# Kernel optimization log

Hardware: AMD Instinct MI355X
Metric: run time of the kernel (lower is better)

## Reference

```python
import jax, jax.numpy as jnp
import numpy as np

E = 1024
H = 16
D = E // H  # head_dim = 64


def setup_inputs() -> dict:
    key = jax.random.key(0)
    k_x, k_w1, k_b1, k_w2, k_b2 = jax.random.split(key, 5)
    s = 1.0 / np.sqrt(E)
    return {
        "x": jax.random.normal(k_x, (2, 2048, E), dtype=jnp.float32),
        "qkv_w": jax.random.uniform(k_w1, (3 * E, E), jnp.float32, -s, s),
        "qkv_b": jax.random.uniform(k_b1, (3 * E,), jnp.float32, -s, s),
        "out_w": jax.random.uniform(k_w2, (E, E), jnp.float32, -s, s),
        "out_b": jax.random.uniform(k_b2, (E,), jnp.float32, -s, s),
    }


def reference(x, qkv_w, qkv_b, out_w, out_b):
    B, T, _ = x.shape
    # qkv projection (torch Linear: x @ W.T + b)
    qkv = x @ qkv_w.T + qkv_b  # [B, T, 3E]
    q, k, v = jnp.split(qkv, 3, axis=-1)
    # [B, T, E] -> [B, H, T, D]
    def to_heads(t):
        return t.reshape(B, T, H, D).transpose(0, 2, 1, 3)
    q, k, v = to_heads(q), to_heads(k), to_heads(v)
    scale = 1.0 / np.sqrt(D).astype(np.float32)
    scores = jnp.einsum("bhqd,bhkd->bhqk", q, k) * scale  # [B, H, T, T]
    attn = jax.nn.softmax(scores, axis=-1)
    # dropout is identity in eval mode
    out = jnp.einsum("bhqk,bhkd->bhqd", attn, v)  # [B, H, T, D]
    out = out.transpose(0, 2, 1, 3).reshape(B, T, E)
    return out @ out_w.T + out_b
```

## Files before the change

kernel.cpp:

```cpp
#include <hip/hip_runtime.h>

#define TT 2048
#define BB 2
#define EE 1024
#define HH 16
#define DD 64
#define E3 3072
#define NTOK 4096

typedef unsigned short u16;
typedef _Float16 __attribute__((ext_vector_type(8))) half8;
typedef _Float16 __attribute__((ext_vector_type(4))) half4;
typedef __fp16 __attribute__((ext_vector_type(2))) fp16x2;
typedef __attribute__((ext_vector_type(4))) float f32x4;

__device__ __forceinline__ unsigned f2h(float f) {
    union { _Float16 h; u16 u; } v; v.h = (_Float16)f; return (unsigned)v.u;
}
__device__ __forceinline__ fp16x2 pk2(float a, float b) {
    return __builtin_amdgcn_cvt_pkrtz(a, b);
}

__device__ __forceinline__ void async_ld16(const u16* g, const u16* l) {
    auto gp = reinterpret_cast<const __attribute__((address_space(1))) unsigned*>(
        reinterpret_cast<uintptr_t>(g));
    auto lp = reinterpret_cast<__attribute__((address_space(3))) unsigned*>(
        reinterpret_cast<uintptr_t>(l));
    __builtin_amdgcn_global_load_lds(gp, lp, 16, 0, 0);
}

__global__ __launch_bounds__(256) void split3(
    const float* __restrict__ x, const float* __restrict__ w1,
    const float* __restrict__ w2,
    u16* __restrict__ xh, u16* __restrict__ w1h, u16* __restrict__ w2h)
{
    const int N1 = (NTOK * EE) / 4;
    const int N2 = N1 + (E3 * EE) / 4;
    int i = blockIdx.x * 256 + threadIdx.x;
    const float* src; u16* dst; int j;
    if (i < N1)      { src = x;  dst = xh;  j = i; }
    else if (i < N2) { src = w1; dst = w1h; j = i - N1; }
    else             { src = w2; dst = w2h; j = i - N2; }
    float4 v = ((const float4*)src)[j];
    *(uint2*)&dst[(size_t)j * 4] = make_uint2(
        f2h(v.x) | (f2h(v.y) << 16), f2h(v.z) | (f2h(v.w) << 16));
}

__global__ __launch_bounds__(256) void vtrans(
    const u16* __restrict__ qkv, u16* __restrict__ vt)
{
    __shared__ u16 L[64][72];
    const int tid = threadIdx.x;
    const int t0 = blockIdx.x * 64;
    const int h  = blockIdx.y;
    const int b  = blockIdx.z;
    const int row = tid >> 2;
    const int c16 = (tid & 3) << 4;

    const u16* src = qkv + (size_t)(b * TT + t0 + row) * E3 + 2 * EE + h * DD + c16;
    *(uint4*)&L[row][c16]     = *(const uint4*)src;
    *(uint4*)&L[row][c16 + 8] = *(const uint4*)(src + 8);
    __syncthreads();

    union { uint4 u[2]; u16 s[16]; } P;
#pragma unroll
    for (int j = 0; j < 16; ++j) P.s[j] = L[c16 + j][row];
    u16* dst = vt + ((size_t)(b * HH + h) * DD + row) * TT + t0 + c16;
    *(uint4*)dst       = P.u[0];
    *(uint4*)(dst + 8) = P.u[1];
}

template <int WMT, bool QSCALE, bool F16OUT>
__global__ __launch_bounds__(256, 3) void gemm_f16(
    const u16* __restrict__ Ag, const u16* __restrict__ Wg,
    const float* __restrict__ bias, void* __restrict__ Cout, int M, int N)
{
    constexpr int BM = WMT * 32;
    constexpr int APASS = BM / 32;
    __shared__ u16 sA[BM * 64];
    __shared__ u16 sB[128 * 64];

    const int tid  = threadIdx.x;
    const int lane = tid & 63;
    const int wave = tid >> 6;
    const int quad = lane >> 4;
    const int l16  = lane & 15;
    const int wm = wave >> 1, wn = wave & 1;
    const int m0 = blockIdx.y * BM;
    const int n0 = blockIdx.x * 128;

    const int srow = tid >> 3;
    const int schk = tid & 7;

    const u16* ag[APASS]; int aldw[APASS];
#pragma unroll
    for (int p = 0; p < APASS; ++p) {
        int row = p * 32 + srow;
        ag[p] = Ag + (size_t)(m0 + row) * EE + ((schk ^ (row & 7)) << 3);
        aldw[p] = (p * 256 + wave * 64) * 8;
    }
    const u16* bg[4]; int bldw[4];
#pragma unroll
    for (int p = 0; p < 4; ++p) {
        int row = p * 32 + srow;
        bg[p] = Wg + (size_t)(n0 + row) * EE + ((schk ^ (row & 7)) << 3);
        bldw[p] = (p * 256 + wave * 64) * 8;
    }

    f32x4 acc[WMT][4];
#pragma unroll
    for (int mt = 0; mt < WMT; ++mt)
#pragma unroll
        for (int nt = 0; nt < 4; ++nt) acc[mt][nt] = (f32x4){0.f, 0.f, 0.f, 0.f};

    for (int k0 = 0; k0 < EE; k0 += 64) {
        __syncthreads();
#pragma unroll
        for (int p = 0; p < APASS; ++p) async_ld16(ag[p] + k0, sA + aldw[p]);
#pragma unroll
        for (int p = 0; p < 4; ++p)    async_ld16(bg[p] + k0, sB + bldw[p]);
        __syncthreads();

        half8 fa[WMT][2], fb[4][2];
#pragma unroll
        for (int mt = 0; mt < WMT; ++mt) {
            int r = wm * (WMT * 16) + mt * 16 + l16;
#pragma unroll
            for (int ks = 0; ks < 2; ++ks)
                fa[mt][ks] = *(const half8*)&sA[r * 64 + (((ks * 4 + quad) ^ (r & 7)) << 3)];
        }
#pragma unroll
        for (int nt = 0; nt < 4; ++nt) {
            int r = wn * 64 + nt * 16 + l16;
#pragma unroll
            for (int ks = 0; ks < 2; ++ks)
                fb[nt][ks] = *(const half8*)&sB[r * 64 + (((ks * 4 + quad) ^ (r & 7)) << 3)];
        }
#pragma unroll
        for (int ks = 0; ks < 2; ++ks)
#pragma unroll
            for (int mt = 0; mt < WMT; ++mt)
#pragma unroll
                for (int nt = 0; nt < 4; ++nt)
                    acc[mt][nt] = __builtin_amdgcn_mfma_f32_16x16x32_f16(
                        fa[mt][ks], fb[nt][ks], acc[mt][nt], 0, 0, 0);
    }

    const float scale = (QSCALE && n0 < EE) ? 0.18033688011112042f : 1.0f;
    float bv[4];
#pragma unroll
    for (int nt = 0; nt < 4; ++nt) bv[nt] = bias[n0 + wn * 64 + nt * 16 + l16];
#pragma unroll
    for (int mt = 0; mt < WMT; ++mt)
#pragma unroll
        for (int nt = 0; nt < 4; ++nt)
#pragma unroll
            for (int r = 0; r < 4; ++r) {
                int rg = m0 + wm * (WMT * 16) + mt * 16 + quad * 4 + r;
                int cg = n0 + wn * 64 + nt * 16 + l16;
                float v = (acc[mt][nt][r] + bv[nt]) * scale;
                if (F16OUT) ((u16*)Cout)[(size_t)rg * N + cg] = (u16)f2h(v);
                else        ((float*)Cout)[(size_t)rg * N + cg] = v;
            }
}

__global__ __launch_bounds__(256, 2) void attn_mfma(
    const u16* __restrict__ qkv, const u16* __restrict__ vt,
    u16* __restrict__ obuf)
{
    __shared__ u16 KB[2][128][64];
    __shared__ u16 VB[2][64][128];

    const int tid  = threadIdx.x;
    const int wave = tid >> 6;
    const int lane = tid & 63;
    const int quad = lane >> 4;
    const int l16  = lane & 15;

    const int q0 = blockIdx.x * 128;
    const int hh = blockIdx.y;
    const int b  = blockIdx.z;

    const int srow  = tid >> 3;
    const int schk  = tid & 7;
    const int vsrow = tid >> 4;
    const int vschk = tid & 15;
    const int ldsw  = wave * 512;

    half8 qb[2][2];
#pragma unroll
    for (int qt = 0; qt < 2; ++qt) {
        int row = q0 + wave * 32 + qt * 16 + l16;
        const u16* qg = qkv + (size_t)(b * TT + row) * E3 + hh * DD;
#pragma unroll
        for (int ks = 0; ks < 2; ++ks)
            qb[qt][ks] = *(const half8*)(qg + ks * 32 + quad * 8);
    }

#pragma unroll
    for (int p = 0; p < 4; ++p) {
        int krow = p * 32 + srow;
        async_ld16(qkv + (size_t)(b * TT + krow) * E3 + EE + hh * DD
                       + ((schk ^ (krow & 7)) << 3),
                   &KB[0][0][0] + p * 2048 + ldsw);
        int vrow = p * 16 + vsrow;
        async_ld16(vt + ((size_t)(b * HH + hh) * DD + vrow) * TT
                      + ((vschk ^ (vrow & 15)) << 3),
                   &VB[0][0][0] + p * 2048 + ldsw);
    }
    __syncthreads();

    const f32x4 Z = {0.f, 0.f, 0.f, 0.f};
    float l_i[2] = {0.f, 0.f};
    f32x4 o[4][2];
#pragma unroll
    for (int dt = 0; dt < 4; ++dt)
#pragma unroll
        for (int qt = 0; qt < 2; ++qt) o[dt][qt] = (f32x4){0.f, 0.f, 0.f, 0.f};

    int cur = 0;
    for (int kt = 0; kt < TT; kt += 128, cur ^= 1) {
        const int ktn = (kt + 128) & (TT - 1);
#pragma unroll
        for (int p = 0; p < 4; ++p) {
            int krow = p * 32 + srow;
            async_ld16(qkv + (size_t)(b * TT + ktn + krow) * E3 + EE + hh * DD
                           + ((schk ^ (krow & 7)) << 3),
                       &KB[cur ^ 1][0][0] + p * 2048 + ldsw);
            int vrow = p * 16 + vsrow;
            async_ld16(vt + ((size_t)(b * HH + hh) * DD + vrow) * TT + ktn
                          + ((vschk ^ (vrow & 15)) << 3),
                       &VB[cur ^ 1][0][0] + p * 2048 + ldsw);
        }

        half4 pb[2][8];
#pragma unroll
        for (int kg = 0; kg < 8; ++kg) {
            int r0 = kg * 16 + l16;
            half8 kf0 = *(const half8*)&KB[cur][r0][((quad)     ^ (r0 & 7)) << 3];
            half8 kf1 = *(const half8*)&KB[cur][r0][((4 + quad) ^ (r0 & 7)) << 3];
#pragma unroll
            for (int qt = 0; qt < 2; ++qt) {
                f32x4 t = __builtin_amdgcn_mfma_f32_16x16x32_f16(kf0, qb[qt][0], Z, 0, 0, 0);
                f32x4 s = __builtin_amdgcn_mfma_f32_16x16x32_f16(kf1, qb[qt][1], t, 0, 0, 0);
                float p0 = __builtin_amdgcn_exp2f(s[0]);
                float p1 = __builtin_amdgcn_exp2f(s[1]);
                float p2 = __builtin_amdgcn_exp2f(s[2]);
                float p3 = __builtin_amdgcn_exp2f(s[3]);
                l_i[qt] += (p0 + p1) + (p2 + p3);
                union { fp16x2 h[2]; half4 v; } u;
                u.h[0] = pk2(p0, p1);
                u.h[1] = pk2(p2, p3);
                pb[qt][kg] = u.v;
            }
        }

#pragma unroll
        for (int kg = 0; kg < 8; ++kg) {
            int c = kg * 2 + (quad >> 1);
#pragma unroll
            for (int dt = 0; dt < 4; ++dt) {
                int vr = dt * 16 + l16;
                half4 vf = *(const half4*)&VB[cur][vr]
                               [((c ^ l16) << 3) + ((quad & 1) << 2)];
                o[dt][0] = __builtin_amdgcn_mfma_f32_16x16x16f16(vf, pb[0][kg], o[dt][0], 0, 0, 0);
                o[dt][1] = __builtin_amdgcn_mfma_f32_16x16x16f16(vf, pb[1][kg], o[dt][1], 0, 0, 0);
            }
        }

        __syncthreads();
    }

    float inv[2];
#pragma unroll
    for (int qt = 0; qt < 2; ++qt) {
        float l = l_i[qt];
        l += __shfl_xor(l, 16, 64);
        l += __shfl_xor(l, 32, 64);
        inv[qt] = 1.f / l;
    }
#pragma unroll
    for (int qt = 0; qt < 2; ++qt) {
        size_t base = (size_t)(b * TT + q0 + wave * 32 + qt * 16 + l16) * EE + hh * DD;
#pragma unroll
        for (int dt = 0; dt < 4; ++dt) {
            unsigned hv[4];
#pragma unroll
            for (int r = 0; r < 4; ++r) hv[r] = f2h(o[dt][qt][r] * inv[qt]);
            *(uint2*)&obuf[base + dt * 16 + quad * 4] =
                make_uint2(hv[0] | (hv[1] << 16), hv[2] | (hv[3] << 16));
        }
    }
}

extern "C" void kernel_launch(void* const* d_in, const int* in_sizes, int n_in,
                              void* d_out, int out_size, void* d_ws, size_t ws_size,
                              hipStream_t stream)
{
    const float* x     = (const float*)d_in[0];
    const float* qkv_w = (const float*)d_in[1];
    const float* qkv_b = (const float*)d_in[2];
    const float* out_w = (const float*)d_in[3];
    const float* out_b = (const float*)d_in[4];
    float* out = (float*)d_out;

    const size_t NX  = (size_t)NTOK * EE;
    const size_t NW1 = (size_t)E3 * EE;
    const size_t NW2 = (size_t)EE * EE;
    const size_t NQ  = (size_t)NTOK * E3;

    u16* ws   = (u16*)d_ws;
    u16* x_h  = ws;
    u16* w1h  = ws + NX;
    u16* w2h  = w1h + NW1;
    u16* qkvb = w2h + NW2;
    u16* vtb  = qkvb + NQ;

    split3<<<dim3((unsigned)((NX + NW1 + NW2) / 4 / 256)), 256, 0, stream>>>(
        x, qkv_w, out_w, x_h, w1h, w2h);

    gemm_f16<4, true, true><<<dim3(E3 / 128, NTOK / 128), 256, 0, stream>>>(
        x_h, w1h, qkv_b, (void*)qkvb, NTOK, E3);

    vtrans<<<dim3(TT / 64, HH, BB), 256, 0, stream>>>(qkvb, vtb);

    attn_mfma<<<dim3(TT / 128, HH, BB), 256, 0, stream>>>(qkvb, vtb, x_h);

    gemm_f16<2, false, false><<<dim3(EE / 128, NTOK / 64), 256, 0, stream>>>(
        x_h, w2h, out_b, (void*)out, NTOK, EE);
}
```

Baseline: 189.5 us.

## Fuse V transpose into QKV GEMM epilogue and add MFMA priority hints

```diff
diff --git a/kernel.cpp b/kernel.cpp
--- a/kernel.cpp
+++ b/kernel.cpp
@@ -16,6 +16,11 @@
 
 __device__ __forceinline__ unsigned f2h(float f) {
     union { _Float16 h; u16 u; } v; v.h = (_Float16)f; return (unsigned)v.u;
+}
+__device__ __forceinline__ unsigned pkh(float a, float b) {
+    union { fp16x2 h; unsigned u; } v;
+    v.h = __builtin_amdgcn_cvt_pkrtz(a, b);
+    return v.u;
 }
 __device__ __forceinline__ fp16x2 pk2(float a, float b) {
     return __builtin_amdgcn_cvt_pkrtz(a, b);
@@ -46,39 +51,17 @@
         f2h(v.x) | (f2h(v.y) << 16), f2h(v.z) | (f2h(v.w) << 16));
 }
 
-__global__ __launch_bounds__(256) void vtrans(
-    const u16* __restrict__ qkv, u16* __restrict__ vt)
-{
-    __shared__ u16 L[64][72];
-    const int tid = threadIdx.x;
-    const int t0 = blockIdx.x * 64;
-    const int h  = blockIdx.y;
-    const int b  = blockIdx.z;
-    const int row = tid >> 2;
-    const int c16 = (tid & 3) << 4;
-
-    const u16* src = qkv + (size_t)(b * TT + t0 + row) * E3 + 2 * EE + h * DD + c16;
-    *(uint4*)&L[row][c16]     = *(const uint4*)src;
-    *(uint4*)&L[row][c16 + 8] = *(const uint4*)(src + 8);
-    __syncthreads();
-
-    union { uint4 u[2]; u16 s[16]; } P;
-#pragma unroll
-    for (int j = 0; j < 16; ++j) P.s[j] = L[c16 + j][row];
-    u16* dst = vt + ((size_t)(b * HH + h) * DD + row) * TT + t0 + c16;
-    *(uint4*)dst       = P.u[0];
-    *(uint4*)(dst + 8) = P.u[1];
-}
-
 template <int WMT, bool QSCALE, bool F16OUT>
 __global__ __launch_bounds__(256, 3) void gemm_f16(
     const u16* __restrict__ Ag, const u16* __restrict__ Wg,
-    const float* __restrict__ bias, void* __restrict__ Cout, int M, int N)
+    const float* __restrict__ bias, void* __restrict__ Cout,
+    u16* __restrict__ vtp, int M, int N)
 {
     constexpr int BM = WMT * 32;
     constexpr int APASS = BM / 32;
-    __shared__ u16 sA[BM * 64];
-    __shared__ u16 sB[128 * 64];
+    __shared__ u16 sAB[(BM + 128) * 64];
+    u16* sA = sAB;
+    u16* sB = sAB + BM * 64;
 
     const int tid  = threadIdx.x;
     const int lane = tid & 63;
@@ -150,6 +133,43 @@
     float bv[4];
 #pragma unroll
     for (int nt = 0; nt < 4; ++nt) bv[nt] = bias[n0 + wn * 64 + nt * 16 + l16];
+
+    if constexpr (F16OUT) {
+        if (vtp != nullptr && n0 >= 2 * EE) {
+            __syncthreads();
+            u16* tile = sAB;
+#pragma unroll
+            for (int mt = 0; mt < WMT; ++mt)
+#pragma unroll
+                for (int nt = 0; nt < 4; ++nt) {
+                    int c  = wn * 64 + nt * 16 + l16;
+                    int ub = (wm * 16 + mt * 4 + quad) ^ ((c & 7) << 1);
+                    *(uint2*)&tile[c * 128 + ub * 4] = make_uint2(
+                        f2h(acc[mt][nt][0] + bv[nt]) | (f2h(acc[mt][nt][1] + bv[nt]) << 16),
+                        f2h(acc[mt][nt][2] + bv[nt]) | (f2h(acc[mt][nt][3] + bv[nt]) << 16));
+                }
+            __syncthreads();
+            const int t8 = tid & 7;
+            const int bq = m0 >> 11;
+            const int tokb = m0 & (TT - 1);
+#pragma unroll
+            for (int p = 0; p < 4; ++p) {
+                int c  = p * 32 + (tid >> 3);
+                int hd = ((n0 - 2 * EE) >> 6) + (c >> 6);
+                int d  = c & 63;
+                u16* dst = vtp + ((size_t)(bq * HH + hd) * DD + d) * TT
+                               + tokb + t8 * 16;
+                int x = (c & 7) << 1;
+#pragma unroll
+                for (int j = 0; j < 2; ++j) {
+                    int u = (t8 * 4 + j * 2) ^ x;
+                    *(uint4*)(dst + j * 8) = *(const uint4*)&tile[c * 128 + u * 4];
+                }
+            }
+            return;
+        }
+    }
+
 #pragma unroll
     for (int mt = 0; mt < WMT; ++mt)
 #pragma unroll
@@ -241,8 +261,10 @@
             half8 kf1 = *(const half8*)&KB[cur][r0][((4 + quad) ^ (r0 & 7)) << 3];
 #pragma unroll
             for (int qt = 0; qt < 2; ++qt) {
+                __builtin_amdgcn_s_setprio(1);
                 f32x4 t = __builtin_amdgcn_mfma_f32_16x16x32_f16(kf0, qb[qt][0], Z, 0, 0, 0);
                 f32x4 s = __builtin_amdgcn_mfma_f32_16x16x32_f16(kf1, qb[qt][1], t, 0, 0, 0);
+                __builtin_amdgcn_s_setprio(0);
                 float p0 = __builtin_amdgcn_exp2f(s[0]);
                 float p1 = __builtin_amdgcn_exp2f(s[1]);
                 float p2 = __builtin_amdgcn_exp2f(s[2]);
@@ -255,6 +277,7 @@
             }
         }
 
+        __builtin_amdgcn_s_setprio(1);
 #pragma unroll
         for (int kg = 0; kg < 8; ++kg) {
             int c = kg * 2 + (quad >> 1);
@@ -267,6 +290,7 @@
                 o[dt][1] = __builtin_amdgcn_mfma_f32_16x16x16f16(vf, pb[1][kg], o[dt][1], 0, 0, 0);
             }
         }
+        __builtin_amdgcn_s_setprio(0);
 
         __syncthreads();
     }
@@ -320,12 +344,10 @@
         x, qkv_w, out_w, x_h, w1h, w2h);
 
     gemm_f16<4, true, true><<<dim3(E3 / 128, NTOK / 128), 256, 0, stream>>>(
-        x_h, w1h, qkv_b, (void*)qkvb, NTOK, E3);
-
-    vtrans<<<dim3(TT / 64, HH, BB), 256, 0, stream>>>(qkvb, vtb);
+        x_h, w1h, qkv_b, (void*)qkvb, vtb, NTOK, E3);
 
     attn_mfma<<<dim3(TT / 128, HH, BB), 256, 0, stream>>>(qkvb, vtb, x_h);
 
     gemm_f16<2, false, false><<<dim3(EE / 128, NTOK / 64), 256, 0, stream>>>(
-        x_h, w2h, out_b, (void*)out, NTOK, EE);
-}
+        x_h, w2h, out_b, (void*)out, nullptr, NTOK, EE);
+}
```

After: 177.7 us. 1.07x faster.
